# Kernel tuning notes

Hardware: AMD Instinct MI355X
Metric: run time of the kernel (lower is better)

## Reference

```python
import jax, jax.numpy as jnp
import numpy as np

B, T, C, H = 4, 2048, 1024, 16
NEG = -1e9  # masked-fill value (finite to keep grads clean)


def setup_inputs() -> dict:
    key = jax.random.key(0)
    ks = jax.random.split(key, 5)
    s = 1.0 / np.sqrt(C)  # keep logits O(1) like trained linear layers
    return {
        "x": jax.random.normal(ks[0], (B, T, C), dtype=jnp.float32),
        "wq": jax.random.normal(ks[1], (C, C), dtype=jnp.float32) * s,
        "bq": jnp.zeros((C,), dtype=jnp.float32),
        "wk": jax.random.normal(ks[2], (C, C), dtype=jnp.float32) * s,
        "bk": jnp.zeros((C,), dtype=jnp.float32),
        "wv": jax.random.normal(ks[3], (C, C), dtype=jnp.float32) * s,
        "bv": jnp.zeros((C,), dtype=jnp.float32),
        "wo": jax.random.normal(ks[4], (C, C), dtype=jnp.float32) * s,
        "bo": jnp.zeros((C,), dtype=jnp.float32),
    }


def _split_heads(y):
    # [B,T,C] -> [B,H,T,hd]
    b, t, c = y.shape
    return y.reshape(b, t, H, c // H).transpose(0, 2, 1, 3)


def reference(x, wq, bq, wk, bk, wv, bv, wo, bo):
    b, t, c = x.shape
    scale = (c // H) ** (-0.5)
    q = _split_heads(x @ wq.T + bq)  # [B,H,T,hd]
    k = _split_heads(x @ wk.T + bk)
    v = _split_heads(x @ wv.T + bv)
    att = jnp.einsum("bhqd,bhkd->bhqk", q, k) * scale  # [B,H,T,T]
    causal = jnp.tril(jnp.ones((t, t), dtype=bool))
    att = jnp.where(causal[None, None], att, NEG)
    att = jax.nn.softmax(att, axis=-1)  # dropout is identity in eval mode
    y = jnp.einsum("bhqk,bhkd->bhqd", att, v)
    y = y.transpose(0, 2, 1, 3).reshape(b, t, c)
    return y @ wo.T + bo
```

## Files before the change

kernel.cpp:

```cpp
#include <hip/hip_runtime.h>


#define B_ 4
#define T_ 2048
#define C_ 1024
#define H_ 16
#define M_ 8192

typedef unsigned short u16;
typedef __bf16 bf16x8 __attribute__((ext_vector_type(8)));
typedef float f32x4 __attribute__((ext_vector_type(4)));

static __device__ __forceinline__ u16 f2bf(float f) {
  unsigned int u = __float_as_uint(f);
  u += 0x7fffu + ((u >> 16) & 1u);
  return (u16)(u >> 16);
}

static __device__ __forceinline__ void async16(const void* g, void* l) {
  __builtin_amdgcn_global_load_lds(
      (const __attribute__((address_space(1))) unsigned int*)g,
      (__attribute__((address_space(3))) unsigned int*)l, 16, 0, 0);
}

#if __has_builtin(__builtin_amdgcn_exp2f)
#define EXP2F(x) __builtin_amdgcn_exp2f(x)
#else
#define EXP2F(x) exp2f(x)
#endif

static __device__ __forceinline__ f32x4 mfma32(bf16x8 a, bf16x8 b, f32x4 c) {
  return __builtin_amdgcn_mfma_f32_16x16x32_bf16(a, b, c, 0, 0, 0);
}

__global__ __launch_bounds__(256) void cvt_all(const float* __restrict__ x,
                                               const float* __restrict__ w0,
                                               const float* __restrict__ w1,
                                               const float* __restrict__ w2,
                                               const float* __restrict__ w3,
                                               u16* __restrict__ xb,
                                               u16* __restrict__ wb,
                                               float s0) {
  const int NX = M_ * C_ / 4, NW = C_ * C_ / 4;
  int i = blockIdx.x * 256 + threadIdx.x;
  const float* src;
  u16* dst;
  int idx;
  float s = 1.f;
  if (i < NX) {
    src = x; dst = xb; idx = i;
  } else {
    int j = i - NX;
    int w = j / NW;
    idx = j - w * NW;
    src = (w == 0) ? w0 : (w == 1) ? w1 : (w == 2) ? w2 : w3;
    dst = wb + (size_t)w * C_ * C_;
    if (w == 0) s = s0;
  }
  float4 f = ((const float4*)src)[idx];
  ushort4 o;
  o.x = f2bf(f.x * s); o.y = f2bf(f.y * s); o.z = f2bf(f.z * s); o.w = f2bf(f.w * s);
  ((ushort4*)dst)[idx] = o;
}

__global__ __launch_bounds__(256) void gemm_qkv(const u16* __restrict__ A,
                                                const u16* __restrict__ W,
                                                const float* __restrict__ bq,
                                                const float* __restrict__ bk,
                                                const float* __restrict__ bv,
                                                float qscale,
                                                u16* __restrict__ outqk,
                                                u16* __restrict__ vtb) {
  __shared__ __align__(16) union {
    struct { u16 A[128 * 64]; u16 B[128 * 64]; } s;
    u16 C[128 * 136];
  } sm;
  const int tid = threadIdx.x, lane = tid & 63, wave = tid >> 6;
  const int quad = lane >> 4, l16 = lane & 15;
  const int wm = wave >> 1, wn = wave & 1;
  const int sel = blockIdx.x >> 3;
  const int col0 = (blockIdx.x & 7) * 128, row0 = blockIdx.y * 128;
  const u16* Bt = W + (size_t)sel * C_ * C_;
  const float* bias = sel == 0 ? bq : (sel == 1 ? bk : bv);
  const float bscale = sel == 0 ? qscale : 1.f;

  f32x4 zero = {0.f, 0.f, 0.f, 0.f};
  f32x4 acc[4][4];
#pragma unroll
  for (int i = 0; i < 4; i++)
#pragma unroll
    for (int j = 0; j < 4; j++) acc[i][j] = zero;

  for (int k0 = 0; k0 < C_; k0 += 64) {
#pragma unroll
    for (int i = 0; i < 4; i++) {
      int c = i * 256 + tid;
      int r = c >> 3, gcc = (c & 7) ^ (r & 7);
      async16(A + (size_t)(row0 + r) * C_ + k0 + gcc * 8,
              sm.s.A + (size_t)(i * 256 + wave * 64) * 8);
      async16(Bt + (size_t)(col0 + r) * C_ + k0 + gcc * 8,
              sm.s.B + (size_t)(i * 256 + wave * 64) * 8);
    }
    __syncthreads();

#pragma unroll
    for (int kk = 0; kk < 2; kk++) {
      bf16x8 a[4], b[4];
#pragma unroll
      for (int i = 0; i < 4; i++) {
        int rm = wm * 64 + 16 * i + l16;
        a[i] = *(const bf16x8*)(sm.s.A + rm * 64 + (((kk * 4 + quad) ^ (rm & 7)) * 8));
        int rn = wn * 64 + 16 * i + l16;
        b[i] = *(const bf16x8*)(sm.s.B + rn * 64 + (((kk * 4 + quad) ^ (rn & 7)) * 8));
      }
#pragma unroll
      for (int i = 0; i < 4; i++)
#pragma unroll
        for (int j = 0; j < 4; j++)
          acc[i][j] = mfma32(a[i], b[j], acc[i][j]);
    }
    __syncthreads();
  }

  float bj[4];
#pragma unroll
  for (int j = 0; j < 4; j++) bj[j] = bias[col0 + wn * 64 + 16 * j + l16] * bscale;

  if (sel == 2) {
#pragma unroll
    for (int i = 0; i < 4; i++)
#pragma unroll
      for (int j = 0; j < 4; j++) {
        int cl = wn * 64 + 16 * j + l16;
        int rt = wm * 64 + 16 * i + quad * 4;
        union { u16 s[4]; uint2 u; } w;
#pragma unroll
        for (int r = 0; r < 4; r++) w.s[r] = f2bf(acc[i][j][r] + bj[j]);
        *(uint2*)(sm.C + (size_t)cl * 136 + rt) = w.u;
      }
    __syncthreads();
    const int bb = row0 >> 11, t0 = row0 & 2047;
#pragma unroll
    for (int c2 = 0; c2 < 8; c2++) {
      int c = c2 * 256 + tid;
      int nr = c >> 4, ch = c & 15;
      bf16x8 v = *(const bf16x8*)(sm.C + (size_t)nr * 136 + ch * 8);
      int gn = col0 + nr, d = gn & 63, hh = gn >> 6;
      *(bf16x8*)(vtb + ((size_t)((bb * 16 + hh) * 64 + d)) * T_ + t0 + ch * 8) = v;
    }
  } else {
#pragma unroll
    for (int i = 0; i < 4; i++)
#pragma unroll
      for (int j = 0; j < 4; j++) {
        int cl = wn * 64 + 16 * j + l16;
        int rt = wm * 64 + 16 * i + quad * 4;
#pragma unroll
        for (int r = 0; r < 4; r++)
          sm.C[(size_t)(rt + r) * 136 + cl] = f2bf(acc[i][j][r] + bj[j]);
      }
    __syncthreads();
    u16* dst = outqk + (size_t)sel * M_ * C_;
#pragma unroll
    for (int c2 = 0; c2 < 8; c2++) {
      int c = c2 * 256 + tid;
      int rw = c >> 4, ch = c & 15;
      bf16x8 v = *(const bf16x8*)(sm.C + (size_t)rw * 136 + ch * 8);
      *(bf16x8*)(dst + (size_t)(row0 + rw) * C_ + col0 + ch * 8) = v;
    }
  }
}

__global__ __launch_bounds__(256) void gemm_o(const u16* __restrict__ A,
                                              const u16* __restrict__ Bt,
                                              const float* __restrict__ bias,
                                              float* __restrict__ outf) {
  __shared__ __align__(16) union {
    struct { u16 A[128 * 64]; u16 B[128 * 64]; } s;
    float Cf[64 * 132];
  } sm;
  const int tid = threadIdx.x, lane = tid & 63, wave = tid >> 6;
  const int quad = lane >> 4, l16 = lane & 15;
  const int wm = wave >> 1, wn = wave & 1;
  const int col0 = blockIdx.x * 128, row0 = blockIdx.y * 128;

  f32x4 zero = {0.f, 0.f, 0.f, 0.f};
  f32x4 acc[4][4];
#pragma unroll
  for (int i = 0; i < 4; i++)
#pragma unroll
    for (int j = 0; j < 4; j++) acc[i][j] = zero;

  for (int k0 = 0; k0 < C_; k0 += 64) {
#pragma unroll
    for (int i = 0; i < 4; i++) {
      int c = i * 256 + tid;
      int r = c >> 3, gcc = (c & 7) ^ (r & 7);
      async16(A + (size_t)(row0 + r) * C_ + k0 + gcc * 8,
              sm.s.A + (size_t)(i * 256 + wave * 64) * 8);
      async16(Bt + (size_t)(col0 + r) * C_ + k0 + gcc * 8,
              sm.s.B + (size_t)(i * 256 + wave * 64) * 8);
    }
    __syncthreads();

#pragma unroll
    for (int kk = 0; kk < 2; kk++) {
      bf16x8 a[4], b[4];
#pragma unroll
      for (int i = 0; i < 4; i++) {
        int rm = wm * 64 + 16 * i + l16;
        a[i] = *(const bf16x8*)(sm.s.A + rm * 64 + (((kk * 4 + quad) ^ (rm & 7)) * 8));
        int rn = wn * 64 + 16 * i + l16;
        b[i] = *(const bf16x8*)(sm.s.B + rn * 64 + (((kk * 4 + quad) ^ (rn & 7)) * 8));
      }
#pragma unroll
      for (int i = 0; i < 4; i++)
#pragma unroll
        for (int j = 0; j < 4; j++)
          acc[i][j] = mfma32(a[i], b[j], acc[i][j]);
    }
    __syncthreads();
  }

  float bj[4];
#pragma unroll
  for (int j = 0; j < 4; j++) bj[j] = bias[col0 + wn * 64 + 16 * j + l16];

#pragma unroll
  for (int cc = 0; cc < 2; cc++) {
    if (cc) __syncthreads();
    if (wm == cc) {
#pragma unroll
      for (int i = 0; i < 4; i++)
#pragma unroll
        for (int j = 0; j < 4; j++) {
          int cl = wn * 64 + 16 * j + l16;
          int rl = 16 * i + quad * 4;
#pragma unroll
          for (int r = 0; r < 4; r++)
            sm.Cf[(size_t)(rl + r) * 132 + cl] = acc[i][j][r] + bj[j];
        }
    }
    __syncthreads();
#pragma unroll
    for (int f2 = 0; f2 < 8; f2++) {
      int f = f2 * 256 + tid;
      int rl = f >> 5, c4 = f & 31;
      float4 v = *(const float4*)(sm.Cf + (size_t)rl * 132 + c4 * 4);
      *(float4*)(outf + (size_t)(row0 + cc * 64 + rl) * C_ + col0 + c4 * 4) = v;
    }
  }
}

__global__ __launch_bounds__(256) void attn(const u16* __restrict__ q,
                                            const u16* __restrict__ k,
                                            const u16* __restrict__ vt,
                                            u16* __restrict__ y) {
  __shared__ __align__(16) u16 Ksm[128 * 64];
  __shared__ __align__(16) u16 Vsm[2][64 * 64];
  __shared__ __align__(16) u16 Psm[4][32 * 64];
  const int tid = threadIdx.x, lane = tid & 63, wave = tid >> 6;
  const int quad = lane >> 4, l16 = lane & 15;
  static const int qperm[16] = {15, 14, 11, 10, 12, 13, 8, 9, 3, 2, 7, 6, 0, 1, 4, 5};
  const int bh = blockIdx.x;
  const int qt = qperm[blockIdx.y];
  const int b = bh >> 4, h = bh & 15;

  bf16x8 qf[2][2];
#pragma unroll
  for (int m = 0; m < 2; m++) {
    const u16* qp =
        q + (size_t)(b * T_ + qt * 128 + wave * 32 + m * 16 + l16) * C_ + h * 64;
#pragma unroll
    for (int ks = 0; ks < 2; ks++)
      qf[m][ks] = *(const bf16x8*)(qp + ks * 32 + quad * 8);
  }

  f32x4 zero = {0.f, 0.f, 0.f, 0.f};
  f32x4 o[2][4];
  float lp[2][4];
#pragma unroll
  for (int m = 0; m < 2; m++) {
#pragma unroll
    for (int dt = 0; dt < 4; dt++) o[m][dt] = zero;
#pragma unroll
    for (int r = 0; r < 4; r++) lp[m][r] = 0.f;
  }

  const u16* kp[4];
  const u16* vp[4];
#pragma unroll
  for (int i = 0; i < 4; i++) {
    int c = i * 256 + tid;
    int r = c >> 3, lc = (c & 7) ^ (r & 7);
    kp[i] = k + (size_t)(b * T_ + r) * C_ + h * 64 + lc * 8;
  }
#pragma unroll
  for (int s = 0; s < 2; s++)
#pragma unroll
    for (int i = 0; i < 2; i++) {
      int c = i * 256 + tid;
      int r = c >> 3, lc = (c & 7) ^ (r & 7);
      vp[s * 2 + i] = vt + (size_t)(bh * 64 + r) * T_ + 64 * s + lc * 8;
    }

  int qrel[2];
#pragma unroll
  for (int m = 0; m < 2; m++)
    qrel[m] = wave * 32 + m * 16 + quad * 4 - l16;

  u16* Pw = &Psm[wave][0];

#pragma unroll 1
  for (int jt = 0; jt <= qt; ++jt) {
#pragma unroll
    for (int i = 0; i < 4; i++) {
      async16(kp[i], Ksm + (size_t)(i * 256 + wave * 64) * 8);
      kp[i] += (size_t)128 * C_;
    }
#pragma unroll
    for (int s = 0; s < 2; s++)
#pragma unroll
      for (int i = 0; i < 2; i++) {
        async16(vp[s * 2 + i], Vsm[s] + (size_t)(i * 256 + wave * 64) * 8);
        vp[s * 2 + i] += 128;
      }
    __syncthreads();

    const bool diag = (jt == qt);
#pragma unroll
    for (int hh = 0; hh < 2; ++hh) {
      if (diag && (2 * wave + 2 - 4 * hh) <= 0) continue;
#pragma unroll
      for (int n = 0; n < 4; ++n) {
        int rk = hh * 64 + n * 16 + l16;
        bf16x8 kf0 = *(const bf16x8*)(Ksm + rk * 64 + ((quad ^ (rk & 7)) * 8));
        bf16x8 kf1 = *(const bf16x8*)(Ksm + rk * 64 + (((4 + quad) ^ (rk & 7)) * 8));
#pragma unroll
        for (int m = 0; m < 2; ++m) {
          int nlim = diag ? (2 * wave + m + 1 - 4 * hh) : 4;
          if (n < nlim) {
            f32x4 s = mfma32(qf[m][0], kf0, zero);
            s = mfma32(qf[m][1], kf1, s);
            float e[4];
#pragma unroll
            for (int r = 0; r < 4; r++) e[r] = EXP2F(s[r]);
            if (diag) {
              int rmin = hh * 64 + n * 16 - qrel[m];
#pragma unroll
              for (int r = 0; r < 4; r++)
                if (r < rmin) e[r] = 0.f;
            }
#pragma unroll
            for (int r = 0; r < 4; r++) {
              lp[m][r] += e[r];
              int qr = m * 16 + quad * 4 + r;
              Pw[qr * 64 + (((n * 2 + (l16 >> 3)) ^ (qr & 7)) * 8) + (l16 & 7)] =
                  f2bf(e[r]);
            }
          } else {
#pragma unroll
            for (int r = 0; r < 4; r++) {
              int qr = m * 16 + quad * 4 + r;
              Pw[qr * 64 + (((n * 2 + (l16 >> 3)) ^ (qr & 7)) * 8) + (l16 & 7)] = 0;
            }
          }
        }
      }
      bf16x8 pf[2][2];
#pragma unroll
      for (int m = 0; m < 2; m++)
#pragma unroll
        for (int ks = 0; ks < 2; ks++)
          pf[m][ks] = *(const bf16x8*)(Pw + (m * 16 + l16) * 64 +
                                       (((ks * 4 + quad) ^ (l16 & 7)) * 8));
#pragma unroll
      for (int dt = 0; dt < 4; ++dt) {
        int rv = dt * 16 + l16;
        bf16x8 vf0 = *(const bf16x8*)(Vsm[hh] + rv * 64 + ((quad ^ (rv & 7)) * 8));
        bf16x8 vf1 = *(const bf16x8*)(Vsm[hh] + rv * 64 + (((4 + quad) ^ (rv & 7)) * 8));
#pragma unroll
        for (int m = 0; m < 2; m++) {
          o[m][dt] = mfma32(pf[m][0], vf0, o[m][dt]);
          o[m][dt] = mfma32(pf[m][1], vf1, o[m][dt]);
        }
      }
    }
    __syncthreads();
  }

#pragma unroll
  for (int m = 0; m < 2; m++)
#pragma unroll
    for (int r = 0; r < 4; r++) {
      float v = lp[m][r];
      v += __shfl_xor(v, 1);
      v += __shfl_xor(v, 2);
      v += __shfl_xor(v, 4);
      v += __shfl_xor(v, 8);
      lp[m][r] = 1.f / v;
    }

#pragma unroll
  for (int m = 0; m < 2; m++)
#pragma unroll
    for (int r = 0; r < 4; r++) {
      int grow = b * T_ + qt * 128 + wave * 32 + m * 16 + quad * 4 + r;
#pragma unroll
      for (int dt = 0; dt < 4; dt++)
        y[(size_t)grow * C_ + h * 64 + dt * 16 + l16] = f2bf(o[m][dt][r] * lp[m][r]);
    }
}

extern "C" void kernel_launch(void* const* d_in, const int* in_sizes, int n_in,
                              void* d_out, int out_size, void* d_ws, size_t ws_size,
                              hipStream_t stream) {
  const float* x  = (const float*)d_in[0];
  const float* wq = (const float*)d_in[1];
  const float* bq = (const float*)d_in[2];
  const float* wk = (const float*)d_in[3];
  const float* bk = (const float*)d_in[4];
  const float* wv = (const float*)d_in[5];
  const float* bv = (const float*)d_in[6];
  const float* wo = (const float*)d_in[7];
  const float* bo = (const float*)d_in[8];
  float* out = (float*)d_out;

  const float QSCALE = 0.125f * 1.4426950408889634f;

  u16* xb  = (u16*)d_ws;
  u16* wqb = xb  + (size_t)M_ * C_;
  u16* wob = wqb + 3 * (size_t)C_ * C_;
  u16* qb  = wob + (size_t)C_ * C_;
  u16* kb  = qb  + (size_t)M_ * C_;
  u16* vtb = kb  + (size_t)M_ * C_;
  u16* yb  = xb;

  const int NCVT = (M_ * C_ + 4 * C_ * C_) / 4 / 256;
  cvt_all<<<NCVT, 256, 0, stream>>>(x, wq, wk, wv, wo, xb, wqb, QSCALE);

  gemm_qkv<<<dim3(24, M_ / 128), 256, 0, stream>>>(xb, wqb, bq, bk, bv, QSCALE,
                                                   qb, vtb);

  attn<<<dim3(B_ * H_, 16), 256, 0, stream>>>(qb, kb, vtb, yb);

  gemm_o<<<dim3(C_ / 128, M_ / 128), 256, 0, stream>>>(yb, wob, bo, out);
}
```

Measured before the change: 261.4 us.

## Triple-buffer QKV and output GEMMs with 256x128 tiles and XCD-aware mapping

Both projection GEMMs now use 512-thread blocks computing 256x128 tiles, with a three-stage async global-to-LDS pipeline controlled by explicit vmcnt waits and raw barriers instead of load-then-sync per k step. Block indices are remapped so that consecutive row tiles land on the same XCD, improving L2 reuse of A rows. MFMA sections are wrapped in s_setprio and split into two halves separated by a barrier. This aims to hide global load latency and cut sync overhead, at the cost of much larger LDS use (about 144KB per block), which limits occupancy and makes the hand-counted waitcnt values fragile.

```diff
diff --git a/kernel.cpp b/kernel.cpp
--- a/kernel.cpp
+++ b/kernel.cpp
@@ -32,6 +32,8 @@
 static __device__ __forceinline__ f32x4 mfma32(bf16x8 a, bf16x8 b, f32x4 c) {
   return __builtin_amdgcn_mfma_f32_16x16x32_bf16(a, b, c, 0, 0, 0);
 }
+
+#define FENCE() asm volatile("" ::: "memory")
 
 __global__ __launch_bounds__(256) void cvt_all(const float* __restrict__ x,
                                                const float* __restrict__ w0,
@@ -63,27 +65,57 @@
   ((ushort4*)dst)[idx] = o;
 }
 
-__global__ __launch_bounds__(256) void gemm_qkv(const u16* __restrict__ A,
-                                                const u16* __restrict__ W,
-                                                const float* __restrict__ bq,
-                                                const float* __restrict__ bk,
-                                                const float* __restrict__ bv,
-                                                float qscale,
-                                                u16* __restrict__ outqk,
-                                                u16* __restrict__ vtb) {
+__global__ __launch_bounds__(512, 2) void gemm_qkv(const u16* __restrict__ A,
+                                                   const u16* __restrict__ W,
+                                                   const float* __restrict__ bq,
+                                                   const float* __restrict__ bk,
+                                                   const float* __restrict__ bv,
+                                                   float qscale,
+                                                   u16* __restrict__ outqk,
+                                                   u16* __restrict__ vtb) {
   __shared__ __align__(16) union {
-    struct { u16 A[128 * 64]; u16 B[128 * 64]; } s;
-    u16 C[128 * 136];
+    u16 buf[3][24576];
+    u16 Cu[256 * 136];
+    u16 Ct[128 * 272];
   } sm;
   const int tid = threadIdx.x, lane = tid & 63, wave = tid >> 6;
   const int quad = lane >> 4, l16 = lane & 15;
   const int wm = wave >> 1, wn = wave & 1;
-  const int sel = blockIdx.x >> 3;
-  const int col0 = (blockIdx.x & 7) * 128, row0 = blockIdx.y * 128;
+  const int bid = blockIdx.x;
+  const int xcd = bid & 7, idx = bid >> 3;
+  const int cq = idx >> 2;
+  const int row0 = (xcd * 4 + (idx & 3)) * 256;
+  const int sel = cq >> 3, colw = cq & 7;
+  const int col0 = colw * 128;
   const u16* Bt = W + (size_t)sel * C_ * C_;
   const float* bias = sel == 0 ? bq : (sel == 1 ? bk : bv);
   const float bscale = sel == 0 ? qscale : 1.f;
 
+  const u16* aptr[4];
+  const u16* bptr[2];
+#pragma unroll
+  for (int it = 0; it < 4; it++) {
+    int c = it * 512 + tid, r = c >> 3, g = (c & 7) ^ (r & 7);
+    aptr[it] = A + (size_t)(row0 + r) * C_ + g * 8;
+  }
+#pragma unroll
+  for (int it = 0; it < 2; it++) {
+    int c = it * 512 + tid, r = c >> 3, g = (c & 7) ^ (r & 7);
+    bptr[it] = Bt + (size_t)(col0 + r) * C_ + g * 8;
+  }
+
+  auto STAGE = [&](int t, int pp) {
+    const int k0 = t * 64;
+    u16* lA = sm.buf[pp];
+    u16* lB = sm.buf[pp] + 16384;
+#pragma unroll
+    for (int it = 0; it < 4; it++)
+      async16(aptr[it] + k0, lA + (size_t)(it * 512 + wave * 64) * 8);
+#pragma unroll
+    for (int it = 0; it < 2; it++)
+      async16(bptr[it] + k0, lB + (size_t)(it * 512 + wave * 64) * 8);
+  };
+
   f32x4 zero = {0.f, 0.f, 0.f, 0.f};
   f32x4 acc[4][4];
 #pragma unroll
@@ -91,36 +123,86 @@
 #pragma unroll
     for (int j = 0; j < 4; j++) acc[i][j] = zero;
 
-  for (int k0 = 0; k0 < C_; k0 += 64) {
-#pragma unroll
-    for (int i = 0; i < 4; i++) {
-      int c = i * 256 + tid;
-      int r = c >> 3, gcc = (c & 7) ^ (r & 7);
-      async16(A + (size_t)(row0 + r) * C_ + k0 + gcc * 8,
-              sm.s.A + (size_t)(i * 256 + wave * 64) * 8);
-      async16(Bt + (size_t)(col0 + r) * C_ + k0 + gcc * 8,
-              sm.s.B + (size_t)(i * 256 + wave * 64) * 8);
-    }
-    __syncthreads();
-
-#pragma unroll
-    for (int kk = 0; kk < 2; kk++) {
-      bf16x8 a[4], b[4];
-#pragma unroll
-      for (int i = 0; i < 4; i++) {
+  STAGE(0, 0);
+  STAGE(1, 1);
+
+  int p = 0, p2 = 2;
+#pragma unroll 1
+  for (int u = 0; u < 16; ++u) {
+    FENCE();
+    __builtin_amdgcn_s_barrier();
+    FENCE();
+    if (u < 14) STAGE(u + 2, p2);
+    if (u < 14) {
+      asm volatile("s_waitcnt vmcnt(12)" ::: "memory");
+    } else if (u < 15) {
+      asm volatile("s_waitcnt vmcnt(6)" ::: "memory");
+    } else {
+      asm volatile("s_waitcnt vmcnt(0)" ::: "memory");
+    }
+    FENCE();
+    __builtin_amdgcn_s_barrier();
+    FENCE();
+
+    const u16* As = sm.buf[p];
+    const u16* Bs = sm.buf[p] + 16384;
+    bf16x8 bfr[4][2];
+#pragma unroll
+    for (int j = 0; j < 4; j++) {
+      int rn = wn * 64 + 16 * j + l16;
+#pragma unroll
+      for (int kk = 0; kk < 2; kk++)
+        bfr[j][kk] =
+            *(const bf16x8*)(Bs + rn * 64 + (((kk * 4 + quad) ^ (rn & 7)) * 8));
+    }
+    {
+      bf16x8 a2[2][2];
+#pragma unroll
+      for (int i = 0; i < 2; i++) {
         int rm = wm * 64 + 16 * i + l16;
-        a[i] = *(const bf16x8*)(sm.s.A + rm * 64 + (((kk * 4 + quad) ^ (rm & 7)) * 8));
-        int rn = wn * 64 + 16 * i + l16;
-        b[i] = *(const bf16x8*)(sm.s.B + rn * 64 + (((kk * 4 + quad) ^ (rn & 7)) * 8));
-      }
-#pragma unroll
-      for (int i = 0; i < 4; i++)
-#pragma unroll
-        for (int j = 0; j < 4; j++)
-          acc[i][j] = mfma32(a[i], b[j], acc[i][j]);
-    }
-    __syncthreads();
-  }
+#pragma unroll
+        for (int kk = 0; kk < 2; kk++)
+          a2[i][kk] =
+              *(const bf16x8*)(As + rm * 64 + (((kk * 4 + quad) ^ (rm & 7)) * 8));
+      }
+      __builtin_amdgcn_s_setprio(1);
+#pragma unroll
+      for (int i = 0; i < 2; i++)
+#pragma unroll
+        for (int j = 0; j < 4; j++) {
+          acc[i][j] = mfma32(a2[i][0], bfr[j][0], acc[i][j]);
+          acc[i][j] = mfma32(a2[i][1], bfr[j][1], acc[i][j]);
+        }
+      __builtin_amdgcn_s_setprio(0);
+    }
+    FENCE();
+    __builtin_amdgcn_s_barrier();
+    FENCE();
+    {
+      bf16x8 a2[2][2];
+#pragma unroll
+      for (int i = 0; i < 2; i++) {
+        int rm = wm * 64 + 16 * (i + 2) + l16;
+#pragma unroll
+        for (int kk = 0; kk < 2; kk++)
+          a2[i][kk] =
+              *(const bf16x8*)(As + rm * 64 + (((kk * 4 + quad) ^ (rm & 7)) * 8));
+      }
+      __builtin_amdgcn_s_setprio(1);
+#pragma unroll
+      for (int i = 0; i < 2; i++)
+#pragma unroll
+        for (int j = 0; j < 4; j++) {
+          acc[i + 2][j] = mfma32(a2[i][0], bfr[j][0], acc[i + 2][j]);
+          acc[i + 2][j] = mfma32(a2[i][1], bfr[j][1], acc[i + 2][j]);
+        }
+      __builtin_amdgcn_s_setprio(0);
+    }
+    asm volatile("s_waitcnt lgkmcnt(0)" ::: "memory");
+    p = (p == 2) ? 0 : p + 1;
+    p2 = (p2 == 2) ? 0 : p2 + 1;
+  }
+  __syncthreads();
 
   float bj[4];
 #pragma unroll
@@ -131,20 +213,20 @@
     for (int i = 0; i < 4; i++)
 #pragma unroll
       for (int j = 0; j < 4; j++) {
-        int cl = wn * 64 + 16 * j + l16;
+        int lc = wn * 64 + 16 * j + l16;
         int rt = wm * 64 + 16 * i + quad * 4;
         union { u16 s[4]; uint2 u; } w;
 #pragma unroll
         for (int r = 0; r < 4; r++) w.s[r] = f2bf(acc[i][j][r] + bj[j]);
-        *(uint2*)(sm.C + (size_t)cl * 136 + rt) = w.u;
+        *(uint2*)(sm.Ct + (size_t)lc * 272 + rt) = w.u;
       }
     __syncthreads();
     const int bb = row0 >> 11, t0 = row0 & 2047;
 #pragma unroll
     for (int c2 = 0; c2 < 8; c2++) {
-      int c = c2 * 256 + tid;
-      int nr = c >> 4, ch = c & 15;
-      bf16x8 v = *(const bf16x8*)(sm.C + (size_t)nr * 136 + ch * 8);
+      int c = c2 * 512 + tid;
+      int nr = c >> 5, ch = c & 31;
+      bf16x8 v = *(const bf16x8*)(sm.Ct + (size_t)nr * 272 + ch * 8);
       int gn = col0 + nr, d = gn & 63, hh = gn >> 6;
       *(bf16x8*)(vtb + ((size_t)((bb * 16 + hh) * 64 + d)) * T_ + t0 + ch * 8) = v;
     }
@@ -153,36 +235,64 @@
     for (int i = 0; i < 4; i++)
 #pragma unroll
       for (int j = 0; j < 4; j++) {
-        int cl = wn * 64 + 16 * j + l16;
+        int lc = wn * 64 + 16 * j + l16;
         int rt = wm * 64 + 16 * i + quad * 4;
 #pragma unroll
         for (int r = 0; r < 4; r++)
-          sm.C[(size_t)(rt + r) * 136 + cl] = f2bf(acc[i][j][r] + bj[j]);
+          sm.Cu[(size_t)(rt + r) * 136 + lc] = f2bf(acc[i][j][r] + bj[j]);
       }
     __syncthreads();
     u16* dst = outqk + (size_t)sel * M_ * C_;
 #pragma unroll
     for (int c2 = 0; c2 < 8; c2++) {
-      int c = c2 * 256 + tid;
+      int c = c2 * 512 + tid;
       int rw = c >> 4, ch = c & 15;
-      bf16x8 v = *(const bf16x8*)(sm.C + (size_t)rw * 136 + ch * 8);
+      bf16x8 v = *(const bf16x8*)(sm.Cu + (size_t)rw * 136 + ch * 8);
       *(bf16x8*)(dst + (size_t)(row0 + rw) * C_ + col0 + ch * 8) = v;
     }
   }
 }
 
-__global__ __launch_bounds__(256) void gemm_o(const u16* __restrict__ A,
-                                              const u16* __restrict__ Bt,
-                                              const float* __restrict__ bias,
-                                              float* __restrict__ outf) {
+__global__ __launch_bounds__(512, 2) void gemm_o(const u16* __restrict__ A,
+                                                 const u16* __restrict__ Bt,
+                                                 const float* __restrict__ bias,
+                                                 float* __restrict__ outf) {
   __shared__ __align__(16) union {
-    struct { u16 A[128 * 64]; u16 B[128 * 64]; } s;
-    float Cf[64 * 132];
+    u16 buf[3][24576];
+    float Cf[256 * 132];
   } sm;
   const int tid = threadIdx.x, lane = tid & 63, wave = tid >> 6;
   const int quad = lane >> 4, l16 = lane & 15;
   const int wm = wave >> 1, wn = wave & 1;
-  const int col0 = blockIdx.x * 128, row0 = blockIdx.y * 128;
+  const int bid = blockIdx.x;
+  const int xcd = bid & 7, idx = bid >> 3;
+  const int row0 = (xcd * 4 + (idx & 3)) * 256;
+  const int col0 = (idx >> 2) * 128;
+
+  const u16* aptr[4];
+  const u16* bptr[2];
+#pragma unroll
+  for (int it = 0; it < 4; it++) {
+    int c = it * 512 + tid, r = c >> 3, g = (c & 7) ^ (r & 7);
+    aptr[it] = A + (size_t)(row0 + r) * C_ + g * 8;
+  }
+#pragma unroll
+  for (int it = 0; it < 2; it++) {
+    int c = it * 512 + tid, r = c >> 3, g = (c & 7) ^ (r & 7);
+    bptr[it] = Bt + (size_t)(col0 + r) * C_ + g * 8;
+  }
+
+  auto STAGE = [&](int t, int pp) {
+    const int k0 = t * 64;
+    u16* lA = sm.buf[pp];
+    u16* lB = sm.buf[pp] + 16384;
+#pragma unroll
+    for (int it = 0; it < 4; it++)
+      async16(aptr[it] + k0, lA + (size_t)(it * 512 + wave * 64) * 8);
+#pragma unroll
+    for (int it = 0; it < 2; it++)
+      async16(bptr[it] + k0, lB + (size_t)(it * 512 + wave * 64) * 8);
+  };
 
   f32x4 zero = {0.f, 0.f, 0.f, 0.f};
   f32x4 acc[4][4];
@@ -191,64 +301,108 @@
 #pragma unroll
     for (int j = 0; j < 4; j++) acc[i][j] = zero;
 
-  for (int k0 = 0; k0 < C_; k0 += 64) {
-#pragma unroll
-    for (int i = 0; i < 4; i++) {
-      int c = i * 256 + tid;
-      int r = c >> 3, gcc = (c & 7) ^ (r & 7);
-      async16(A + (size_t)(row0 + r) * C_ + k0 + gcc * 8,
-              sm.s.A + (size_t)(i * 256 + wave * 64) * 8);
-      async16(Bt + (size_t)(col0 + r) * C_ + k0 + gcc * 8,
-              sm.s.B + (size_t)(i * 256 + wave * 64) * 8);
-    }
-    __syncthreads();
-
-#pragma unroll
-    for (int kk = 0; kk < 2; kk++) {
-      bf16x8 a[4], b[4];
-#pragma unroll
-      for (int i = 0; i < 4; i++) {
+  STAGE(0, 0);
+  STAGE(1, 1);
+
+  int p = 0, p2 = 2;
+#pragma unroll 1
+  for (int u = 0; u < 16; ++u) {
+    FENCE();
+    __builtin_amdgcn_s_barrier();
+    FENCE();
+    if (u < 14) STAGE(u + 2, p2);
+    if (u < 14) {
+      asm volatile("s_waitcnt vmcnt(12)" ::: "memory");
+    } else if (u < 15) {
+      asm volatile("s_waitcnt vmcnt(6)" ::: "memory");
+    } else {
+      asm volatile("s_waitcnt vmcnt(0)" ::: "memory");
+    }
+    FENCE();
+    __builtin_amdgcn_s_barrier();
+    FENCE();
+
+    const u16* As = sm.buf[p];
+    const u16* Bs = sm.buf[p] + 16384;
+    bf16x8 bfr[4][2];
+#pragma unroll
+    for (int j = 0; j < 4; j++) {
+      int rn = wn * 64 + 16 * j + l16;
+#pragma unroll
+      for (int kk = 0; kk < 2; kk++)
+        bfr[j][kk] =
+            *(const bf16x8*)(Bs + rn * 64 + (((kk * 4 + quad) ^ (rn & 7)) * 8));
+    }
+    {
+      bf16x8 a2[2][2];
+#pragma unroll
+      for (int i = 0; i < 2; i++) {
         int rm = wm * 64 + 16 * i + l16;
-        a[i] = *(const bf16x8*)(sm.s.A + rm * 64 + (((kk * 4 + quad) ^ (rm & 7)) * 8));
-        int rn = wn * 64 + 16 * i + l16;
-        b[i] = *(const bf16x8*)(sm.s.B + rn * 64 + (((kk * 4 + quad) ^ (rn & 7)) * 8));
-      }
-#pragma unroll
-      for (int i = 0; i < 4; i++)
-#pragma unroll
-        for (int j = 0; j < 4; j++)
-          acc[i][j] = mfma32(a[i], b[j], acc[i][j]);
-    }
-    __syncthreads();
-  }
+#pragma unroll
+        for (int kk = 0; kk < 2; kk++)
+          a2[i][kk] =
+              *(const bf16x8*)(As + rm * 64 + (((kk * 4 + quad) ^ (rm & 7)) * 8));
+      }
+      __builtin_amdgcn_s_setprio(1);
+#pragma unroll
+      for (int i = 0; i < 2; i++)
+#pragma unroll
+        for (int j = 0; j < 4; j++) {
+          acc[i][j] = mfma32(a2[i][0], bfr[j][0], acc[i][j]);
+          acc[i][j] = mfma32(a2[i][1], bfr[j][1], acc[i][j]);
+        }
+      __builtin_amdgcn_s_setprio(0);
+    }
+    FENCE();
+    __builtin_amdgcn_s_barrier();
+    FENCE();
+    {
+      bf16x8 a2[2][2];
+#pragma unroll
+      for (int i = 0; i < 2; i++) {
+        int rm = wm * 64 + 16 * (i + 2) + l16;
+#pragma unroll
+        for (int kk = 0; kk < 2; kk++)
+          a2[i][kk] =
+              *(const bf16x8*)(As + rm * 64 + (((kk * 4 + quad) ^ (rm & 7)) * 8));
+      }
+      __builtin_amdgcn_s_setprio(1);
+#pragma unroll
+      for (int i = 0; i < 2; i++)
+#pragma unroll
+        for (int j = 0; j < 4; j++) {
+          acc[i + 2][j] = mfma32(a2[i][0], bfr[j][0], acc[i + 2][j]);
+          acc[i + 2][j] = mfma32(a2[i][1], bfr[j][1], acc[i + 2][j]);
+        }
+      __builtin_amdgcn_s_setprio(0);
+    }
+    asm volatile("s_waitcnt lgkmcnt(0)" ::: "memory");
+    p = (p == 2) ? 0 : p + 1;
+    p2 = (p2 == 2) ? 0 : p2 + 1;
+  }
+  __syncthreads();
 
   float bj[4];
 #pragma unroll
   for (int j = 0; j < 4; j++) bj[j] = bias[col0 + wn * 64 + 16 * j + l16];
 
 #pragma unroll
-  for (int cc = 0; cc < 2; cc++) {
-    if (cc) __syncthreads();
-    if (wm == cc) {
-#pragma unroll
-      for (int i = 0; i < 4; i++)
-#pragma unroll
-        for (int j = 0; j < 4; j++) {
-          int cl = wn * 64 + 16 * j + l16;
-          int rl = 16 * i + quad * 4;
-#pragma unroll
-          for (int r = 0; r < 4; r++)
-            sm.Cf[(size_t)(rl + r) * 132 + cl] = acc[i][j][r] + bj[j];
-        }
-    }
-    __syncthreads();
-#pragma unroll
-    for (int f2 = 0; f2 < 8; f2++) {
-      int f = f2 * 256 + tid;
-      int rl = f >> 5, c4 = f & 31;
-      float4 v = *(const float4*)(sm.Cf + (size_t)rl * 132 + c4 * 4);
-      *(float4*)(outf + (size_t)(row0 + cc * 64 + rl) * C_ + col0 + c4 * 4) = v;
-    }
+  for (int i = 0; i < 4; i++)
+#pragma unroll
+    for (int j = 0; j < 4; j++) {
+      int lc = wn * 64 + 16 * j + l16;
+      int rt = wm * 64 + 16 * i + quad * 4;
+#pragma unroll
+      for (int r = 0; r < 4; r++)
+        sm.Cf[(size_t)(rt + r) * 132 + lc] = acc[i][j][r] + bj[j];
+    }
+  __syncthreads();
+#pragma unroll
+  for (int c2 = 0; c2 < 16; c2++) {
+    int c = c2 * 512 + tid;
+    int rw = c >> 5, c4 = c & 31;
+    float4 v = *(const float4*)(sm.Cf + (size_t)rw * 132 + c4 * 4);
+    *(float4*)(outf + (size_t)(row0 + rw) * C_ + col0 + c4 * 4) = v;
   }
 }
 
@@ -439,10 +593,9 @@
   const int NCVT = (M_ * C_ + 4 * C_ * C_) / 4 / 256;
   cvt_all<<<NCVT, 256, 0, stream>>>(x, wq, wk, wv, wo, xb, wqb, QSCALE);
 
-  gemm_qkv<<<dim3(24, M_ / 128), 256, 0, stream>>>(xb, wqb, bq, bk, bv, QSCALE,
-                                                   qb, vtb);
+  gemm_qkv<<<768, 512, 0, stream>>>(xb, wqb, bq, bk, bv, QSCALE, qb, vtb);
 
   attn<<<dim3(B_ * H_, 16), 256, 0, stream>>>(qb, kb, vtb, yb);
 
-  gemm_o<<<dim3(C_ / 128, M_ / 128), 256, 0, stream>>>(yb, wob, bo, out);
-}
+  gemm_o<<<256, 512, 0, stream>>>(yb, wob, bo, out);
+}
```

New measurement: 263.1 us. About the same (+0.6%).
